# Performance work log

Measured on AMD Instinct MI355X. Metric: run time of the kernel, lower is better.

Reference implementation:

```python
import jax, jax.numpy as jnp
import numpy as np
from jax import lax

K_NN = 20          # cfg.nsample
BN_EPS = 1e-5


def fps(xyz, npoint, farthest0):
    """Furthest point sampling. xyz: [B,N,3] -> idx [B,npoint] (int)."""
    B, N, _ = xyz.shape

    def step(carry, _):
        distance, far = carry                                  # [B,N], [B]
        centroid = jnp.take_along_axis(xyz, far[:, None, None], axis=1)  # [B,1,3]
        d = jnp.sum((xyz - centroid) ** 2, axis=-1)            # [B,N]
        distance = jnp.minimum(distance, d)
        new_far = jnp.argmax(distance, axis=-1)
        return (distance, new_far), far

    init = (jnp.full((B, N), 1e10, dtype=xyz.dtype), farthest0)
    (_, _), idxs = lax.scan(step, init, None, length=npoint)   # idxs: [npoint,B]
    return jnp.transpose(idxs)                                 # [B,npoint]


def setup_inputs() -> dict:
    key = jax.random.key(0)
    k1, k2, k3, k4 = jax.random.split(key, 4)
    B, N, C = 4, 8192, 128
    c_in = C * 2 + 6   # mlps[0]*2 + 6 (use_xyz) = 262
    c_out = 256
    xyz = jax.random.normal(k1, (B, N, 3), dtype=jnp.float32)
    feat = jax.random.normal(k2, (B, N, C), dtype=jnp.float32)
    conv_w = jax.random.normal(k3, (c_in, c_out), dtype=jnp.float32) * 0.05  # 1x1 conv
    bn_gamma = jnp.ones((c_out,), dtype=jnp.float32)
    bn_beta = jnp.zeros((c_out,), dtype=jnp.float32)
    init_farthest = jax.random.randint(k4, (B,), 0, N)
    return {"xyz": xyz, "feat": feat, "conv_w": conv_w, "bn_gamma": bn_gamma,
            "bn_beta": bn_beta, "init_farthest": init_farthest, "npoints": 2048}


def reference(xyz, feat, conv_w, bn_gamma, bn_beta, init_farthest, npoints):
    # --- FPS sampling ---
    sample_idx = fps(xyz, npoints, init_farthest)                      # [B,S]
    new_xyz = jnp.take_along_axis(xyz, sample_idx[:, :, None], axis=1)  # [B,S,3]

    # --- augment features with xyz (use_xyz=True) ---
    feat_aug = jnp.concatenate([feat, xyz], axis=-1)                   # [B,N,131]
    new_feat_aug = jnp.take_along_axis(feat_aug, sample_idx[:, :, None], axis=1)  # [B,S,131]

    # --- KNN of new_xyz in xyz (squared L2, ascending) ---
    d2 = (jnp.sum(new_xyz ** 2, -1)[:, :, None]
          - 2.0 * jnp.einsum('bsd,bnd->bsn', new_xyz, xyz)
          + jnp.sum(xyz ** 2, -1)[:, None, :])                         # [B,S,N]
    _, knn_idx = lax.top_k(-d2, K_NN)                                  # [B,S,K]

    # --- gather neighbor features, build edge features ---
    knn_feat = jax.vmap(lambda f, i: f[i])(feat_aug, knn_idx)          # [B,S,K,131]
    center = new_feat_aug[:, :, None, :]                               # [B,S,1,131]
    edge = jnp.concatenate(
        [knn_feat - center, jnp.broadcast_to(center, knn_feat.shape)], axis=-1)  # [B,S,K,262]

    # --- shared MLP: 1x1 conv + BN (batch stats) + ReLU ---
    h = jnp.einsum('bskc,co->bsko', edge, conv_w)                      # [B,S,K,256]
    mean = jnp.mean(h, axis=(0, 1, 2))
    var = jnp.var(h, axis=(0, 1, 2))
    h = (h - mean) * lax.rsqrt(var + BN_EPS) * bn_gamma + bn_beta
    h = jax.nn.relu(h)

    # --- max-pool over K neighbors ---
    new_feat = jnp.max(h, axis=2)                                      # [B,S,256]
    return (new_xyz, new_feat, sample_idx)
```

## Files before the change

kernel.cpp:

```cpp
#include <hip/hip_runtime.h>
#include <hip/hip_bf16.h>


#define NPTS   8192
#define NSAMP  2048
#define KNN    20

typedef unsigned long long u64;
typedef unsigned int u32;
typedef unsigned short u16;

template<int CTRL, int RM>
__device__ __forceinline__ u64 dpp_kmax(u64 k) {
  unsigned lo = (unsigned)k, hi = (unsigned)(k >> 32);
  unsigned lo2 = (unsigned)__builtin_amdgcn_update_dpp((int)lo, (int)lo, CTRL, RM, 0xf, false);
  unsigned hi2 = (unsigned)__builtin_amdgcn_update_dpp((int)hi, (int)hi, CTRL, RM, 0xf, false);
  u64 o = ((u64)hi2 << 32) | lo2;
  return o > k ? o : k;
}
template<int CTRL, int RM>
__device__ __forceinline__ u64 dpp_kmin(u64 k) {
  unsigned lo = (unsigned)k, hi = (unsigned)(k >> 32);
  unsigned lo2 = (unsigned)__builtin_amdgcn_update_dpp((int)lo, (int)lo, CTRL, RM, 0xf, false);
  unsigned hi2 = (unsigned)__builtin_amdgcn_update_dpp((int)hi, (int)hi, CTRL, RM, 0xf, false);
  u64 o = ((u64)hi2 << 32) | lo2;
  return o < k ? o : k;
}
template<int CTRL, int RM>
__device__ __forceinline__ float dpp_fmax(float x) {
  int t = __builtin_amdgcn_update_dpp(__float_as_int(x), __float_as_int(x), CTRL, RM, 0xf, false);
  return fmaxf(x, __int_as_float(t));
}
template<int CTRL, int RM>
__device__ __forceinline__ float dpp_fmin(float x) {
  int t = __builtin_amdgcn_update_dpp(__float_as_int(x), __float_as_int(x), CTRL, RM, 0xf, false);
  return fminf(x, __int_as_float(t));
}
__device__ __forceinline__ u64 umax64(u64 a, u64 b) { return a > b ? a : b; }

__device__ __forceinline__ float wave_fmax_bcast(float x) {
  x = dpp_fmax<0xB1, 0xf>(x); x = dpp_fmax<0x4E, 0xf>(x);
  x = dpp_fmax<0x124, 0xf>(x); x = dpp_fmax<0x128, 0xf>(x);
  x = dpp_fmax<0x142, 0xa>(x); x = dpp_fmax<0x143, 0xc>(x);
  return __int_as_float(__builtin_amdgcn_readlane(__float_as_int(x), 63));
}
__device__ __forceinline__ float wave_fmin_bcast(float x) {
  x = dpp_fmin<0xB1, 0xf>(x); x = dpp_fmin<0x4E, 0xf>(x);
  x = dpp_fmin<0x124, 0xf>(x); x = dpp_fmin<0x128, 0xf>(x);
  x = dpp_fmin<0x142, 0xa>(x); x = dpp_fmin<0x143, 0xc>(x);
  return __int_as_float(__builtin_amdgcn_readlane(__float_as_int(x), 63));
}

__device__ __forceinline__ unsigned mspread4(unsigned q) {
  return (q & 1u) | ((q & 2u) << 2) | ((q & 4u) << 4) | ((q & 8u) << 6);
}

__global__ __launch_bounds__(1024, 1) void fps_kernel(
    const float* __restrict__ xyz, const int* __restrict__ farthest0,
    int* __restrict__ sample_int, float* __restrict__ out) {
  __shared__ float sxs[NPTS], sys[NPTS], szs[NPTS];
  __shared__ u16   sidxr[NPTS];
  __shared__ u32   s_samp[NSAMP];
  __shared__ u32   hist[4096];
  __shared__ u32   part[1024];
  __shared__ u64   slot[3];
  __shared__ int   s_isp;
  const int b = blockIdx.x, tid = threadIdx.x, lane = tid & 63;
  const float* xb = xyz + (size_t)b * NPTS * 3;

  for (int i = tid; i < 4096; i += 1024) hist[i] = 0u;
  if (tid < 3) slot[tid] = 0ull;
  __syncthreads();

  float ox[8], oy[8], oz[8];
  int cell[8];
#pragma unroll
  for (int j = 0; j < 8; ++j) {
    int p = tid * 8 + j;
    float x = xb[3*p], y = xb[3*p+1], z = xb[3*p+2];
    ox[j] = x; oy[j] = y; oz[j] = z;
    unsigned qx = (unsigned)(int)fminf(fmaxf((x + 5.2f) * 1.5384615f, 0.f), 15.f);
    unsigned qy = (unsigned)(int)fminf(fmaxf((y + 5.2f) * 1.5384615f, 0.f), 15.f);
    unsigned qz = (unsigned)(int)fminf(fmaxf((z + 5.2f) * 1.5384615f, 0.f), 15.f);
    cell[j] = (int)(mspread4(qx) | (mspread4(qy) << 1) | (mspread4(qz) << 2));
    atomicAdd(&hist[cell[j]], 1u);
  }
  __syncthreads();

  u32 h0 = hist[4*tid], h1 = hist[4*tid+1], h2 = hist[4*tid+2], h3 = hist[4*tid+3];
  u32 mysum = h0 + h1 + h2 + h3;
  part[tid] = mysum;
  __syncthreads();
  for (int off = 1; off < 1024; off <<= 1) {
    u32 u = (tid >= off) ? part[tid - off] : 0u;
    u32 v = part[tid];
    __syncthreads();
    part[tid] = u + v;
    __syncthreads();
  }
  u32 base = part[tid] - mysum;
  hist[4*tid]   = base;
  hist[4*tid+1] = base + h0;
  hist[4*tid+2] = base + h0 + h1;
  hist[4*tid+3] = base + h0 + h1 + h2;
  __syncthreads();

#pragma unroll
  for (int j = 0; j < 8; ++j) {
    u32 p = atomicAdd(&hist[cell[j]], 1u);
    sxs[p] = ox[j]; sys[p] = oy[j]; szs[p] = oz[j];
    sidxr[p] = (u16)(tid * 8 + j);
  }
  __syncthreads();

  const int cur0 = farthest0[b];
#pragma unroll
  for (int j = 0; j < 8; ++j) {
    int p = tid * 8 + j;
    if ((int)sidxr[p] == cur0) s_isp = p;
  }

  float px[8], py[8], pz[8], dist[8];
  u32 low26[8];
#pragma unroll
  for (int j = 0; j < 8; ++j) {
    int p = tid * 8 + j;
    px[j] = sxs[p]; py[j] = sys[p]; pz[j] = szs[p];
    low26[j] = (((~(u32)sidxr[p]) & 0x1FFFu) << 13) | (u32)p;
    dist[j] = 1e10f;
  }
  float lxmin = px[0], lxmax = px[0], lymin = py[0], lymax = py[0], lzmin = pz[0], lzmax = pz[0];
#pragma unroll
  for (int j = 1; j < 8; ++j) {
    lxmin = fminf(lxmin, px[j]); lxmax = fmaxf(lxmax, px[j]);
    lymin = fminf(lymin, py[j]); lymax = fmaxf(lymax, py[j]);
    lzmin = fminf(lzmin, pz[j]); lzmax = fmaxf(lzmax, pz[j]);
  }
  const float wxmin = wave_fmin_bcast(lxmin), wxmax = wave_fmax_bcast(lxmax);
  const float wymin = wave_fmin_bcast(lymin), wymax = wave_fmax_bcast(lymax);
  const float wzmin = wave_fmin_bcast(lzmin), wzmax = wave_fmax_bcast(lzmax);

  u64 kw = ((u64)__float_as_uint(1e10f) << 26);
  __syncthreads();

  int cur_sp = s_isp;
  u32 cur_pack = ((u32)cur0 << 13) | (u32)cur_sp;

  for (int it = 0; it < NSAMP; ++it) {
    if (tid == 0) s_samp[it] = cur_pack;
    if (it == NSAMP - 1) break;
    if (tid == 64) slot[(it+2)%3] = 0ull;
    float cx = sxs[cur_sp], cy = sys[cur_sp], cz = szs[cur_sp];

    float gx = fmaxf(fmaxf(__fsub_rn(wxmin, cx), __fsub_rn(cx, wxmax)), 0.f);
    float gy = fmaxf(fmaxf(__fsub_rn(wymin, cy), __fsub_rn(cy, wymax)), 0.f);
    float gz = fmaxf(fmaxf(__fsub_rn(wzmin, cz), __fsub_rn(cz, wzmax)), 0.f);
    float bound = __fadd_rn(__fadd_rn(__fmul_rn(gx,gx), __fmul_rn(gy,gy)), __fmul_rn(gz,gz));
    float ub = __uint_as_float((u32)(kw >> 26));
    if (!(__fmul_rn(bound, 0.999999f) >= ub)) {
#pragma unroll
      for (int j = 0; j < 8; ++j) {
        float dx = __fsub_rn(px[j], cx);
        float dy = __fsub_rn(py[j], cy);
        float dz = __fsub_rn(pz[j], cz);
        float d  = __fadd_rn(__fadd_rn(__fmul_rn(dx,dx), __fmul_rn(dy,dy)), __fmul_rn(dz,dz));
        dist[j] = fminf(dist[j], d);
      }
      u64 k0 = ((u64)__float_as_uint(dist[0]) << 26) | low26[0];
      u64 k1 = ((u64)__float_as_uint(dist[1]) << 26) | low26[1];
      u64 k2 = ((u64)__float_as_uint(dist[2]) << 26) | low26[2];
      u64 k3 = ((u64)__float_as_uint(dist[3]) << 26) | low26[3];
      u64 k4 = ((u64)__float_as_uint(dist[4]) << 26) | low26[4];
      u64 k5 = ((u64)__float_as_uint(dist[5]) << 26) | low26[5];
      u64 k6 = ((u64)__float_as_uint(dist[6]) << 26) | low26[6];
      u64 k7 = ((u64)__float_as_uint(dist[7]) << 26) | low26[7];
      u64 k = umax64(umax64(umax64(k0,k1), umax64(k2,k3)),
                     umax64(umax64(k4,k5), umax64(k6,k7)));
      k = dpp_kmax<0xB1, 0xf>(k);
      k = dpp_kmax<0x4E, 0xf>(k);
      k = dpp_kmax<0x124, 0xf>(k);
      k = dpp_kmax<0x128, 0xf>(k);
      k = dpp_kmax<0x142, 0xa>(k);
      k = dpp_kmax<0x143, 0xc>(k);
      unsigned klo = (unsigned)__builtin_amdgcn_readlane((int)(unsigned)k, 63);
      unsigned khi = (unsigned)__builtin_amdgcn_readlane((int)(unsigned)(k >> 32), 63);
      kw = ((u64)khi << 32) | klo;
    }
    if (lane == 63) atomicMax(&slot[(it+1)%3], kw);
    __syncthreads();
    u64 wk = slot[(it+1)%3];
    cur_sp = (int)(wk & 0x1FFFu);
    u32 org = (~(u32)(wk >> 13)) & 0x1FFFu;
    cur_pack = (org << 13) | (u32)cur_sp;
  }

  __syncthreads();
  float* outxyz = out + (size_t)b * NSAMP * 3;
  float* outidx = out + 24576 + 2097152 + (size_t)b * NSAMP;
  for (int it = tid; it < NSAMP; it += 1024) {
    u32 s = s_samp[it];
    int org = (int)(s >> 13), sp = (int)(s & 0x1FFFu);
    sample_int[(b << 11) + it] = org;
    outidx[it] = (float)org;
    outxyz[3*it]   = sxs[sp];
    outxyz[3*it+1] = sys[sp];
    outxyz[3*it+2] = szs[sp];
  }
}

__global__ __launch_bounds__(256, 1) void knn_kernel(
    const float* __restrict__ xyz, const int* __restrict__ sample_int,
    int* __restrict__ knn_out) {
  __shared__ u64 lists[4][2][KNN];
  const int tid  = threadIdx.x;
  const int lane = tid & 63, w = tid >> 6;
  const int qq   = blockIdx.x * 4 + w;
  const int b    = qq >> 11;
  const float* xb = xyz + (size_t)b * NPTS * 3;
  const int sidx = sample_int[qq];
  const float sx = xb[3*sidx], sy = xb[3*sidx+1], sz = xb[3*sidx+2];
  const float sqs = __fadd_rn(__fadd_rn(__fmul_rn(sx,sx), __fmul_rn(sy,sy)), __fmul_rn(sz,sz));

  for (int ch = 0; ch < 2; ++ch) {
    const int pbase = ch * 4096;
    float d[64];
#pragma unroll
    for (int i = 0; i < 64; ++i) {
      int p = pbase + i*64 + lane;
      float x = xb[3*p], y = xb[3*p+1], z = xb[3*p+2];
      float dot = __fadd_rn(__fadd_rn(__fmul_rn(sx,x), __fmul_rn(sy,y)), __fmul_rn(sz,z));
      float sqx = __fadd_rn(__fadd_rn(__fmul_rn(x,x), __fmul_rn(y,y)), __fmul_rn(z,z));
      d[i] = __fadd_rn(__fsub_rn(sqs, __fmul_rn(2.0f, dot)), sqx);
    }
    u64 msk = 0ull;
    for (int kk = 0; kk < KNN; ++kk) {
      float bv = 1e30f; int bs = 0;
#pragma unroll
      for (int i = 0; i < 64; ++i) {
        float dc = (msk & (1ull << i)) ? 1e30f : d[i];
        if (dc < bv) { bv = dc; bs = i; }
      }
      unsigned gi = (unsigned)(pbase + bs*64 + lane);
      u64 key = ((u64)__float_as_uint(bv) << 32) | gi;
      key = dpp_kmin<0xB1, 0xf>(key);
      key = dpp_kmin<0x4E, 0xf>(key);
      key = dpp_kmin<0x124, 0xf>(key);
      key = dpp_kmin<0x128, 0xf>(key);
      key = dpp_kmin<0x142, 0xa>(key);
      key = dpp_kmin<0x143, 0xc>(key);
      unsigned glo = (unsigned)__builtin_amdgcn_readlane((int)(unsigned)key, 63);
      unsigned ghi = (unsigned)__builtin_amdgcn_readlane((int)(unsigned)(key >> 32), 63);
      if (lane == (int)(glo & 63u)) msk |= 1ull << ((glo - pbase) >> 6);
      if (lane == 0) lists[w][ch][kk] = ((u64)ghi << 32) | glo;
    }
  }
  u64 mykey = ~0ull; int rank = 64;
  if (lane < 40) {
    int li = lane >= 20 ? 1 : 0;
    int e  = li ? lane - 20 : lane;
    mykey = lists[w][li][e];
    int cnt = e;
    const u64* oth = &lists[w][li ^ 1][0];
#pragma unroll
    for (int j = 0; j < KNN; ++j) cnt += (oth[j] < mykey) ? 1 : 0;
    rank = cnt;
  }
  if (rank < KNN) knn_out[(size_t)qq * KNN + rank] = (int)(mykey & 0xFFFFFFFFull);
}

__global__ void wdiff_kernel(const float* __restrict__ W, float* __restrict__ Wd) {
  int i = blockIdx.x * 256 + threadIdx.x;
  Wd[i] = W[131*256 + i] - W[i];
}

template<bool BF16OUT>
__global__ __launch_bounds__(128) void matmul131_kernel(
    const float* __restrict__ featb, const float* __restrict__ xyzb,
    const int* __restrict__ gidx,
    const float* __restrict__ W, void* __restrict__ outp) {
  __shared__ float tile[32][132];
  const int tid = threadIdx.x;
  const int r0  = blockIdx.x << 5;
  for (int i = tid; i < 32*131; i += 128) {
    int r = i / 131;
    int k = i - r*131;
    int row = r0 + r;
    int src;
    if (gidx) { int bb = row >> 11; src = (bb << 13) + gidx[row]; }
    else      { src = row; }
    float v = (k < 128) ? featb[(size_t)src*128 + k]
                        : xyzb[(size_t)src*3 + (k-128)];
    tile[r][k] = v;
  }
  __syncthreads();
  float acc0[32], acc1[32];
#pragma unroll
  for (int r = 0; r < 32; ++r) { acc0[r] = 0.f; acc1[r] = 0.f; }
  const int c0 = tid, c1 = tid + 128;
  for (int k = 0; k < 128; k += 4) {
    float w00 = W[(k+0)*256+c0], w01 = W[(k+1)*256+c0], w02 = W[(k+2)*256+c0], w03 = W[(k+3)*256+c0];
    float w10 = W[(k+0)*256+c1], w11 = W[(k+1)*256+c1], w12 = W[(k+2)*256+c1], w13 = W[(k+3)*256+c1];
#pragma unroll
    for (int r = 0; r < 32; ++r) {
      float4 a = *(const float4*)&tile[r][k];
      acc0[r] = fmaf(a.x, w00, acc0[r]); acc0[r] = fmaf(a.y, w01, acc0[r]);
      acc0[r] = fmaf(a.z, w02, acc0[r]); acc0[r] = fmaf(a.w, w03, acc0[r]);
      acc1[r] = fmaf(a.x, w10, acc1[r]); acc1[r] = fmaf(a.y, w11, acc1[r]);
      acc1[r] = fmaf(a.z, w12, acc1[r]); acc1[r] = fmaf(a.w, w13, acc1[r]);
    }
  }
#pragma unroll
  for (int kk = 128; kk < 131; ++kk) {
    float w0 = W[kk*256+c0], w1 = W[kk*256+c1];
#pragma unroll
    for (int r = 0; r < 32; ++r) {
      float a = tile[r][kk];
      acc0[r] = fmaf(a, w0, acc0[r]);
      acc1[r] = fmaf(a, w1, acc1[r]);
    }
  }
#pragma unroll
  for (int r = 0; r < 32; ++r) {
    if (BF16OUT) {
      __hip_bfloat16* o = (__hip_bfloat16*)outp;
      o[(size_t)(r0+r)*256 + c0] = __float2bfloat16(acc0[r]);
      o[(size_t)(r0+r)*256 + c1] = __float2bfloat16(acc1[r]);
    } else {
      float* o = (float*)outp;
      o[(size_t)(r0+r)*256 + c0] = acc0[r];
      o[(size_t)(r0+r)*256 + c1] = acc1[r];
    }
  }
}

__global__ __launch_bounds__(256) void stats_kernel(
    const __hip_bfloat16* __restrict__ Pb,
    const int* __restrict__ knn, float* __restrict__ outFeat,
    float* __restrict__ psum, float* __restrict__ psq, int qq0, int prow) {
  const int c = threadIdx.x;
  float s = 0.f, s2 = 0.f;
  const int q0 = qq0 + blockIdx.x * 16;
  for (int q = 0; q < 16; ++q) {
    int qq = q0 + q;
    float qc = outFeat[(size_t)qq*256 + c];
    float m = -1e30f;
    const int* kn = knn + (size_t)qq * KNN;
#pragma unroll
    for (int k = 0; k < KNN; ++k) {
      int idx = kn[k];
      float v = __bfloat162float(Pb[(size_t)idx*256 + c]) + qc;
      m = fmaxf(m, v);
      s += v;
      s2 = fmaf(v, v, s2);
    }
    outFeat[(size_t)qq*256 + c] = m;
  }
  psum[(size_t)(prow + blockIdx.x)*256 + c] = s;
  psq [(size_t)(prow + blockIdx.x)*256 + c] = s2;
}

__global__ __launch_bounds__(256) void reduce_stats_kernel(
    const float* __restrict__ psum, const float* __restrict__ psq,
    const float* __restrict__ gamma, const float* __restrict__ beta,
    float* __restrict__ ss) {
  const int c = blockIdx.x, t = threadIdx.x;
  float s  = psum[(size_t)t*256 + c] + psum[(size_t)(t+256)*256 + c];
  float s2 = psq [(size_t)t*256 + c] + psq [(size_t)(t+256)*256 + c];
#pragma unroll
  for (int off = 32; off >= 1; off >>= 1) {
    s  += __shfl_xor(s,  off);
    s2 += __shfl_xor(s2, off);
  }
  __shared__ float as[4], as2[4];
  const int lane = t & 63, wid = t >> 6;
  if (lane == 0) { as[wid] = s; as2[wid] = s2; }
  __syncthreads();
  if (t == 0) {
    float S  = (as[0]+as[1]) + (as[2]+as[3]);
    float S2 = (as2[0]+as2[1]) + (as2[2]+as2[3]);
    const float inv = 1.f / 163840.f;
    float mean = S * inv;
    float var  = S2 * inv - mean * mean;
    float sc = rsqrtf(var + 1e-5f) * gamma[c];
    ss[c]       = sc;
    ss[256 + c] = beta[c] - mean * sc;
  }
}

__global__ __launch_bounds__(256) void finalize_kernel(
    float* __restrict__ f, const float* __restrict__ ss) {
  int e = blockIdx.x * 256 + threadIdx.x;
  float v = fmaf(f[e], ss[threadIdx.x], ss[256 + threadIdx.x]);
  f[e] = v > 0.f ? v : 0.f;
}

extern "C" void kernel_launch(void* const* d_in, const int* in_sizes, int n_in,
                              void* d_out, int out_size, void* d_ws, size_t ws_size,
                              hipStream_t stream) {
  const float* xyz      = (const float*)d_in[0];
  const float* feat     = (const float*)d_in[1];
  const float* conv_w   = (const float*)d_in[2];
  const float* bn_gamma = (const float*)d_in[3];
  const float* bn_beta  = (const float*)d_in[4];
  const int*   far0     = (const int*)d_in[5];

  char* ws = (char*)d_ws;
  int*   sample_int = (int*)  (ws + 0);
  int*   knn        = (int*)  (ws + 32768);
  float* Wd         = (float*)(ws + 688128);
  float* psum       = (float*)(ws + 822272);
  float* psq        = (float*)(ws + 1346560);
  float* ss         = (float*)(ws + 1870848);
  __hip_bfloat16* Pb = (__hip_bfloat16*)(ws + 2097152);

  float* out     = (float*)d_out;
  float* outFeat = out + 24576;

  fps_kernel  <<<dim3(4),    dim3(1024), 0, stream>>>(xyz, far0, sample_int, out);
  knn_kernel  <<<dim3(2048), dim3(256),  0, stream>>>(xyz, sample_int, knn);
  wdiff_kernel<<<dim3(131),  dim3(256),  0, stream>>>(conv_w, Wd);

  matmul131_kernel<false><<<dim3(256), dim3(128), 0, stream>>>(
      feat, xyz, sample_int, Wd, (void*)outFeat);

  for (int b = 0; b < 4; ++b) {
    matmul131_kernel<true><<<dim3(256), dim3(128), 0, stream>>>(
        feat + (size_t)b*NPTS*128, xyz + (size_t)b*NPTS*3,
        (const int*)nullptr, conv_w, (void*)Pb);
    stats_kernel<<<dim3(128), dim3(256), 0, stream>>>(
        Pb, knn + (size_t)b*NSAMP*KNN, outFeat + (size_t)b*NSAMP*256,
        psum, psq, 0, b*128);
  }

  reduce_stats_kernel<<<dim3(256), dim3(256), 0, stream>>>(psum, psq, bn_gamma, bn_beta, ss);
  finalize_kernel   <<<dim3(8192), dim3(256), 0, stream>>>(outFeat, ss);
}
```

Baseline: 2.332 ms.

## Use per-lane bounding-box culling in FPS and split KNN halves across waves

In the FPS loop, culling now uses each lane's own bounding box of its 8 points and its own running max key instead of wave-wide bounds. Only live lanes recompute distances, and the wave reduction is skipped only when no lane is live, so culling can fire more often. The KNN kernel gives each of the two 4096-point halves of a query its own wave and doubles the grid, merging the halves after a block barrier. This adds parallelism but pays a sync, and one wave per query sits idle during the merge.

```diff
diff --git a/kernel.cpp b/kernel.cpp
--- a/kernel.cpp
+++ b/kernel.cpp
@@ -26,30 +26,7 @@
   u64 o = ((u64)hi2 << 32) | lo2;
   return o < k ? o : k;
 }
-template<int CTRL, int RM>
-__device__ __forceinline__ float dpp_fmax(float x) {
-  int t = __builtin_amdgcn_update_dpp(__float_as_int(x), __float_as_int(x), CTRL, RM, 0xf, false);
-  return fmaxf(x, __int_as_float(t));
-}
-template<int CTRL, int RM>
-__device__ __forceinline__ float dpp_fmin(float x) {
-  int t = __builtin_amdgcn_update_dpp(__float_as_int(x), __float_as_int(x), CTRL, RM, 0xf, false);
-  return fminf(x, __int_as_float(t));
-}
 __device__ __forceinline__ u64 umax64(u64 a, u64 b) { return a > b ? a : b; }
-
-__device__ __forceinline__ float wave_fmax_bcast(float x) {
-  x = dpp_fmax<0xB1, 0xf>(x); x = dpp_fmax<0x4E, 0xf>(x);
-  x = dpp_fmax<0x124, 0xf>(x); x = dpp_fmax<0x128, 0xf>(x);
-  x = dpp_fmax<0x142, 0xa>(x); x = dpp_fmax<0x143, 0xc>(x);
-  return __int_as_float(__builtin_amdgcn_readlane(__float_as_int(x), 63));
-}
-__device__ __forceinline__ float wave_fmin_bcast(float x) {
-  x = dpp_fmin<0xB1, 0xf>(x); x = dpp_fmin<0x4E, 0xf>(x);
-  x = dpp_fmin<0x124, 0xf>(x); x = dpp_fmin<0x128, 0xf>(x);
-  x = dpp_fmin<0x142, 0xa>(x); x = dpp_fmin<0x143, 0xc>(x);
-  return __int_as_float(__builtin_amdgcn_readlane(__float_as_int(x), 63));
-}
 
 __device__ __forceinline__ unsigned mspread4(unsigned q) {
   return (q & 1u) | ((q & 2u) << 2) | ((q & 4u) << 4) | ((q & 8u) << 6);
@@ -136,11 +113,9 @@
     lymin = fminf(lymin, py[j]); lymax = fmaxf(lymax, py[j]);
     lzmin = fminf(lzmin, pz[j]); lzmax = fmaxf(lzmax, pz[j]);
   }
-  const float wxmin = wave_fmin_bcast(lxmin), wxmax = wave_fmax_bcast(lxmax);
-  const float wymin = wave_fmin_bcast(lymin), wymax = wave_fmax_bcast(lymax);
-  const float wzmin = wave_fmin_bcast(lzmin), wzmax = wave_fmax_bcast(lzmax);
-
-  u64 kw = ((u64)__float_as_uint(1e10f) << 26);
+
+  u64 klane = ((u64)__float_as_uint(1e10f) << 26);
+  u64 kw    = ((u64)__float_as_uint(1e10f) << 26);
   __syncthreads();
 
   int cur_sp = s_isp;
@@ -152,39 +127,42 @@
     if (tid == 64) slot[(it+2)%3] = 0ull;
     float cx = sxs[cur_sp], cy = sys[cur_sp], cz = szs[cur_sp];
 
-    float gx = fmaxf(fmaxf(__fsub_rn(wxmin, cx), __fsub_rn(cx, wxmax)), 0.f);
-    float gy = fmaxf(fmaxf(__fsub_rn(wymin, cy), __fsub_rn(cy, wymax)), 0.f);
-    float gz = fmaxf(fmaxf(__fsub_rn(wzmin, cz), __fsub_rn(cz, wzmax)), 0.f);
+    float gx = fmaxf(fmaxf(__fsub_rn(lxmin, cx), __fsub_rn(cx, lxmax)), 0.f);
+    float gy = fmaxf(fmaxf(__fsub_rn(lymin, cy), __fsub_rn(cy, lymax)), 0.f);
+    float gz = fmaxf(fmaxf(__fsub_rn(lzmin, cz), __fsub_rn(cz, lzmax)), 0.f);
     float bound = __fadd_rn(__fadd_rn(__fmul_rn(gx,gx), __fmul_rn(gy,gy)), __fmul_rn(gz,gz));
-    float ub = __uint_as_float((u32)(kw >> 26));
-    if (!(__fmul_rn(bound, 0.999999f) >= ub)) {
-#pragma unroll
-      for (int j = 0; j < 8; ++j) {
-        float dx = __fsub_rn(px[j], cx);
-        float dy = __fsub_rn(py[j], cy);
-        float dz = __fsub_rn(pz[j], cz);
-        float d  = __fadd_rn(__fadd_rn(__fmul_rn(dx,dx), __fmul_rn(dy,dy)), __fmul_rn(dz,dz));
-        dist[j] = fminf(dist[j], d);
+    float ub = __uint_as_float((u32)(klane >> 26));
+    bool live = !(__fmul_rn(bound, 0.999999f) >= ub);
+
+    if (__any(live)) {
+      if (live) {
+#pragma unroll
+        for (int j = 0; j < 8; ++j) {
+          float dx = __fsub_rn(px[j], cx);
+          float dy = __fsub_rn(py[j], cy);
+          float dz = __fsub_rn(pz[j], cz);
+          float d  = __fadd_rn(__fadd_rn(__fmul_rn(dx,dx), __fmul_rn(dy,dy)), __fmul_rn(dz,dz));
+          dist[j] = fminf(dist[j], d);
+        }
+        u64 k0 = ((u64)__float_as_uint(dist[0]) << 26) | low26[0];
+        u64 k1 = ((u64)__float_as_uint(dist[1]) << 26) | low26[1];
+        u64 k2 = ((u64)__float_as_uint(dist[2]) << 26) | low26[2];
+        u64 k3 = ((u64)__float_as_uint(dist[3]) << 26) | low26[3];
+        u64 k4 = ((u64)__float_as_uint(dist[4]) << 26) | low26[4];
+        u64 k5 = ((u64)__float_as_uint(dist[5]) << 26) | low26[5];
+        u64 k6 = ((u64)__float_as_uint(dist[6]) << 26) | low26[6];
+        u64 k7 = ((u64)__float_as_uint(dist[7]) << 26) | low26[7];
+        klane = umax64(umax64(umax64(k0,k1), umax64(k2,k3)),
+                       umax64(umax64(k4,k5), umax64(k6,k7)));
       }
-      u64 k0 = ((u64)__float_as_uint(dist[0]) << 26) | low26[0];
-      u64 k1 = ((u64)__float_as_uint(dist[1]) << 26) | low26[1];
-      u64 k2 = ((u64)__float_as_uint(dist[2]) << 26) | low26[2];
-      u64 k3 = ((u64)__float_as_uint(dist[3]) << 26) | low26[3];
-      u64 k4 = ((u64)__float_as_uint(dist[4]) << 26) | low26[4];
-      u64 k5 = ((u64)__float_as_uint(dist[5]) << 26) | low26[5];
-      u64 k6 = ((u64)__float_as_uint(dist[6]) << 26) | low26[6];
-      u64 k7 = ((u64)__float_as_uint(dist[7]) << 26) | low26[7];
-      u64 k = umax64(umax64(umax64(k0,k1), umax64(k2,k3)),
-                     umax64(umax64(k4,k5), umax64(k6,k7)));
+      u64 k = klane;
       k = dpp_kmax<0xB1, 0xf>(k);
       k = dpp_kmax<0x4E, 0xf>(k);
       k = dpp_kmax<0x124, 0xf>(k);
       k = dpp_kmax<0x128, 0xf>(k);
       k = dpp_kmax<0x142, 0xa>(k);
       k = dpp_kmax<0x143, 0xc>(k);
-      unsigned klo = (unsigned)__builtin_amdgcn_readlane((int)(unsigned)k, 63);
-      unsigned khi = (unsigned)__builtin_amdgcn_readlane((int)(unsigned)(k >> 32), 63);
-      kw = ((u64)khi << 32) | klo;
+      kw = k;
     }
     if (lane == 63) atomicMax(&slot[(it+1)%3], kw);
     __syncthreads();
@@ -211,61 +189,64 @@
 __global__ __launch_bounds__(256, 1) void knn_kernel(
     const float* __restrict__ xyz, const int* __restrict__ sample_int,
     int* __restrict__ knn_out) {
-  __shared__ u64 lists[4][2][KNN];
+  __shared__ u64 lists[2][2][KNN];
   const int tid  = threadIdx.x;
   const int lane = tid & 63, w = tid >> 6;
-  const int qq   = blockIdx.x * 4 + w;
+  const int ql   = w >> 1;
+  const int ch   = w & 1;
+  const int qq   = blockIdx.x * 2 + ql;
   const int b    = qq >> 11;
   const float* xb = xyz + (size_t)b * NPTS * 3;
   const int sidx = sample_int[qq];
   const float sx = xb[3*sidx], sy = xb[3*sidx+1], sz = xb[3*sidx+2];
   const float sqs = __fadd_rn(__fadd_rn(__fmul_rn(sx,sx), __fmul_rn(sy,sy)), __fmul_rn(sz,sz));
 
-  for (int ch = 0; ch < 2; ++ch) {
-    const int pbase = ch * 4096;
-    float d[64];
+  const int pbase = ch * 4096;
+  float d[64];
+#pragma unroll
+  for (int i = 0; i < 64; ++i) {
+    int p = pbase + i*64 + lane;
+    float x = xb[3*p], y = xb[3*p+1], z = xb[3*p+2];
+    float dot = __fadd_rn(__fadd_rn(__fmul_rn(sx,x), __fmul_rn(sy,y)), __fmul_rn(sz,z));
+    float sqx = __fadd_rn(__fadd_rn(__fmul_rn(x,x), __fmul_rn(y,y)), __fmul_rn(z,z));
+    d[i] = __fadd_rn(__fsub_rn(sqs, __fmul_rn(2.0f, dot)), sqx);
+  }
+  u64 msk = 0ull;
+  for (int kk = 0; kk < KNN; ++kk) {
+    float bv = 1e30f; int bs = 0;
 #pragma unroll
     for (int i = 0; i < 64; ++i) {
-      int p = pbase + i*64 + lane;
-      float x = xb[3*p], y = xb[3*p+1], z = xb[3*p+2];
-      float dot = __fadd_rn(__fadd_rn(__fmul_rn(sx,x), __fmul_rn(sy,y)), __fmul_rn(sz,z));
-      float sqx = __fadd_rn(__fadd_rn(__fmul_rn(x,x), __fmul_rn(y,y)), __fmul_rn(z,z));
-      d[i] = __fadd_rn(__fsub_rn(sqs, __fmul_rn(2.0f, dot)), sqx);
-    }
-    u64 msk = 0ull;
-    for (int kk = 0; kk < KNN; ++kk) {
-      float bv = 1e30f; int bs = 0;
-#pragma unroll
-      for (int i = 0; i < 64; ++i) {
-        float dc = (msk & (1ull << i)) ? 1e30f : d[i];
-        if (dc < bv) { bv = dc; bs = i; }
-      }
-      unsigned gi = (unsigned)(pbase + bs*64 + lane);
-      u64 key = ((u64)__float_as_uint(bv) << 32) | gi;
-      key = dpp_kmin<0xB1, 0xf>(key);
-      key = dpp_kmin<0x4E, 0xf>(key);
-      key = dpp_kmin<0x124, 0xf>(key);
-      key = dpp_kmin<0x128, 0xf>(key);
-      key = dpp_kmin<0x142, 0xa>(key);
-      key = dpp_kmin<0x143, 0xc>(key);
-      unsigned glo = (unsigned)__builtin_amdgcn_readlane((int)(unsigned)key, 63);
-      unsigned ghi = (unsigned)__builtin_amdgcn_readlane((int)(unsigned)(key >> 32), 63);
-      if (lane == (int)(glo & 63u)) msk |= 1ull << ((glo - pbase) >> 6);
-      if (lane == 0) lists[w][ch][kk] = ((u64)ghi << 32) | glo;
-    }
-  }
-  u64 mykey = ~0ull; int rank = 64;
-  if (lane < 40) {
-    int li = lane >= 20 ? 1 : 0;
-    int e  = li ? lane - 20 : lane;
-    mykey = lists[w][li][e];
-    int cnt = e;
-    const u64* oth = &lists[w][li ^ 1][0];
-#pragma unroll
-    for (int j = 0; j < KNN; ++j) cnt += (oth[j] < mykey) ? 1 : 0;
-    rank = cnt;
-  }
-  if (rank < KNN) knn_out[(size_t)qq * KNN + rank] = (int)(mykey & 0xFFFFFFFFull);
+      float dc = (msk & (1ull << i)) ? 1e30f : d[i];
+      if (dc < bv) { bv = dc; bs = i; }
+    }
+    unsigned gi = (unsigned)(pbase + bs*64 + lane);
+    u64 key = ((u64)__float_as_uint(bv) << 32) | gi;
+    key = dpp_kmin<0xB1, 0xf>(key);
+    key = dpp_kmin<0x4E, 0xf>(key);
+    key = dpp_kmin<0x124, 0xf>(key);
+    key = dpp_kmin<0x128, 0xf>(key);
+    key = dpp_kmin<0x142, 0xa>(key);
+    key = dpp_kmin<0x143, 0xc>(key);
+    unsigned glo = (unsigned)__builtin_amdgcn_readlane((int)(unsigned)key, 63);
+    unsigned ghi = (unsigned)__builtin_amdgcn_readlane((int)(unsigned)(key >> 32), 63);
+    if (lane == (int)(glo & 63u)) msk |= 1ull << ((glo - pbase) >> 6);
+    if (lane == 0) lists[ql][ch][kk] = ((u64)ghi << 32) | glo;
+  }
+  __syncthreads();
+  if (ch == 0) {
+    u64 mykey = ~0ull; int rank = 64;
+    if (lane < 40) {
+      int li = lane >= 20 ? 1 : 0;
+      int e  = li ? lane - 20 : lane;
+      mykey = lists[ql][li][e];
+      int cnt = e;
+      const u64* oth = &lists[ql][li ^ 1][0];
+#pragma unroll
+      for (int j = 0; j < KNN; ++j) cnt += (oth[j] < mykey) ? 1 : 0;
+      rank = cnt;
+    }
+    if (rank < KNN) knn_out[(size_t)qq * KNN + rank] = (int)(mykey & 0xFFFFFFFFull);
+  }
 }
 
 __global__ void wdiff_kernel(const float* __restrict__ W, float* __restrict__ Wd) {
@@ -417,7 +398,7 @@
   float* outFeat = out + 24576;
 
   fps_kernel  <<<dim3(4),    dim3(1024), 0, stream>>>(xyz, far0, sample_int, out);
-  knn_kernel  <<<dim3(2048), dim3(256),  0, stream>>>(xyz, sample_int, knn);
+  knn_kernel  <<<dim3(4096), dim3(256),  0, stream>>>(xyz, sample_int, knn);
   wdiff_kernel<<<dim3(131),  dim3(256),  0, stream>>>(conv_w, Wd);
 
   matmul131_kernel<false><<<dim3(256), dim3(128), 0, stream>>>(
```

Result: faster. 2.242 ms (-3.9%).
